# Kernel optimization log

Hardware: AMD Instinct MI355X
Metric: run time of the kernel (lower is better)

## Reference

```python
import jax, jax.numpy as jnp
import numpy as np


def setup_inputs() -> dict:
    key = jax.random.key(0)
    k1, k2 = jax.random.split(key)
    B, H, W, C = 8, 192, 640, 64
    c1 = jax.random.normal(k1, (B, H, W, C), dtype=jnp.float32)
    warp = jax.random.normal(k2, (B, H, W, C), dtype=jnp.float32)
    return {"c1": c1, "warp": warp, "search_range": 2}


def reference(c1, warp, search_range):
    # c1, warp: [B, H, W, C]; pad warp along width by search_range on both sides
    padded = jnp.pad(warp, ((0, 0), (0, 0), (search_range, search_range), (0, 0)))
    width = c1.shape[2]
    max_offset = 2 * search_range + 1  # small fixed loop (5 offsets)
    cost_vol = [
        jnp.mean(c1 * padded[:, :, i:width + i, :], axis=3, keepdims=True)
        for i in range(max_offset)
    ]
    # cost_curve: [B, H, W, C + max_offset]
    return jnp.concatenate([c1] + cost_vol, axis=3)
```

## Files before the change

### kernel.cpp

```cpp
#include <hip/hip_runtime.h>


typedef float f32x4 __attribute__((ext_vector_type(4)));

#define WIDTH 640
#define CH 64
#define NOFF 5
#define OUTC 69
#define GPX 4
#define REC_F4 ((GPX * OUTC) / 4)
#define NPIX (8 * 192 * 640)
#define NGROUPS (NPIX / GPX)
#define BDIM 256
#define WPB (BDIM / 64)
#define GPW 2
#define NBLOCKS (NGROUPS / (WPB * GPW))
#define GROUPS_PER_ROW (WIDTH / GPX)

__device__ __forceinline__ float row_reduce_sum16_lane0(float v) {
    union { float f; int i; } a, b;
    a.f = v;
    b.i = __builtin_amdgcn_update_dpp(0, a.i, 0x101, 0xF, 0xF, true); a.f += b.f;
    b.i = __builtin_amdgcn_update_dpp(0, a.i, 0x102, 0xF, 0xF, true); a.f += b.f;
    b.i = __builtin_amdgcn_update_dpp(0, a.i, 0x104, 0xF, 0xF, true); a.f += b.f;
    b.i = __builtin_amdgcn_update_dpp(0, a.i, 0x108, 0xF, 0xF, true); a.f += b.f;
    return a.f;
}

__global__ __launch_bounds__(BDIM) void StereoCostVolume_kernel(
    const float* __restrict__ c1,
    const float* __restrict__ warp,
    float* __restrict__ out)
{
    __shared__ f32x4 lds[WPB * GPW * REC_F4];

    const int t   = threadIdx.x;
    const int wid = t >> 6;
    const int l   = t & 63;
    const int px  = l >> 4;
    const int c4  = l & 15;

    const f32x4* c1f4   = (const f32x4*)c1;
    const f32x4* warpf4 = (const f32x4*)warp;
    f32x4*       outf4  = (f32x4*)out;

    const int gwave = blockIdx.x * WPB + wid;
    const int g0    = gwave * GPW;
    const int row   = g0 / GROUPS_PER_ROW;
    const int gw0   = g0 - row * GROUPS_PER_ROW;

    const int w0 = gw0 * GPX + px;
    const int i0 = (g0 * GPX + px) * 16 + c4;
    const int wb0 = (row * WIDTH + w0) * 16 + c4;

    const f32x4 a0 = __builtin_nontemporal_load(&c1f4[i0]);
    const f32x4 a1 = __builtin_nontemporal_load(&c1f4[i0 + GPX * 16]);

    f32x4 b0[NOFF], b1[NOFF];
    if (gw0 != 0 && gw0 != GROUPS_PER_ROW - 2) {
        #pragma unroll
        for (int d = 0; d < NOFF; ++d) {
            b0[d] = warpf4[wb0 + (d - 2) * 16];
            b1[d] = warpf4[wb0 + (d - 2) * 16 + GPX * 16];
        }
    } else {
        #pragma unroll
        for (int d = 0; d < NOFF; ++d) {
            const int ww0 = w0 + d - 2;
            const int ww1 = ww0 + GPX;
            b0[d] = (ww0 >= 0 && ww0 < WIDTH) ? warpf4[wb0 + (d - 2) * 16]
                                              : f32x4{0.f, 0.f, 0.f, 0.f};
            b1[d] = (ww1 >= 0 && ww1 < WIDTH) ? warpf4[wb0 + (d - 2) * 16 + GPX * 16]
                                              : f32x4{0.f, 0.f, 0.f, 0.f};
        }
    }

    float s0[NOFF], s1[NOFF];
    #pragma unroll
    for (int d = 0; d < NOFF; ++d) {
        const float acc0 = a0.x * b0[d].x + a0.y * b0[d].y + a0.z * b0[d].z + a0.w * b0[d].w;
        const float acc1 = a1.x * b1[d].x + a1.y * b1[d].y + a1.z * b1[d].z + a1.w * b1[d].w;
        s0[d] = row_reduce_sum16_lane0(acc0);
        s1[d] = row_reduce_sum16_lane0(acc1);
    }

    float* rec0 = (float*)&lds[(wid * GPW + 0) * REC_F4];
    float* rec1 = (float*)&lds[(wid * GPW + 1) * REC_F4];
    const int fb = px * OUTC + c4 * 4;
    rec0[fb + 0] = a0.x; rec0[fb + 1] = a0.y; rec0[fb + 2] = a0.z; rec0[fb + 3] = a0.w;
    rec1[fb + 0] = a1.x; rec1[fb + 1] = a1.y; rec1[fb + 2] = a1.z; rec1[fb + 3] = a1.w;
    if (c4 == 0) {
        #pragma unroll
        for (int d = 0; d < NOFF; ++d) {
            rec0[px * OUTC + CH + d] = s0[d] * 0.015625f;
            rec1[px * OUTC + CH + d] = s1[d] * 0.015625f;
        }
    }
    __builtin_amdgcn_wave_barrier();

    {
        const f32x4* r0 = (const f32x4*)rec0;
        const f32x4* r1 = (const f32x4*)rec1;
        const int ob0 = g0 * REC_F4;
        __builtin_nontemporal_store(r0[l], &outf4[ob0 + l]);
        __builtin_nontemporal_store(r1[l], &outf4[ob0 + REC_F4 + l]);
        if (l < REC_F4 - 64) {
            __builtin_nontemporal_store(r0[64 + l], &outf4[ob0 + 64 + l]);
            __builtin_nontemporal_store(r1[64 + l], &outf4[ob0 + REC_F4 + 64 + l]);
        }
    }
}

extern "C" void kernel_launch(void* const* d_in, const int* in_sizes, int n_in,
                              void* d_out, int out_size, void* d_ws, size_t ws_size,
                              hipStream_t stream) {
    const float* c1   = (const float*)d_in[0];
    const float* warp = (const float*)d_in[1];
    float* out = (float*)d_out;

    StereoCostVolume_kernel<<<NBLOCKS, BDIM, 0, stream>>>(c1, warp, out);
}
```

Measured before the change: 126.6 us.

## Make each wave process eight pixel pairs with double-buffered register prefetch

Each wave now loops over eight consecutive 8-pixel groups instead of handling one. It keeps two register fragments so the loads for the next group are issued while the current group is reduced and stored through LDS. The aim is to hide global load latency and amortise per-wave setup and index math. The cost is an eighth of the blocks, which may reduce memory-level parallelism and occupancy, and more registers per thread.

```diff
diff --git a/kernel.cpp b/kernel.cpp
--- a/kernel.cpp
+++ b/kernel.cpp
@@ -7,15 +7,14 @@
 #define CH 64
 #define NOFF 5
 #define OUTC 69
-#define GPX 4
-#define REC_F4 ((GPX * OUTC) / 4)
+#define REC_F4 69
 #define NPIX (8 * 192 * 640)
-#define NGROUPS (NPIX / GPX)
+#define NPAIR (NPIX / 8)
+#define NITER 8
 #define BDIM 256
 #define WPB (BDIM / 64)
-#define GPW 2
-#define NBLOCKS (NGROUPS / (WPB * GPW))
-#define GROUPS_PER_ROW (WIDTH / GPX)
+#define NBLOCKS (NPAIR / (WPB * NITER))
+#define PAIRS_PER_ROW (WIDTH / 8)
 
 __device__ __forceinline__ float row_reduce_sum16_lane0(float v) {
     union { float f; int i; } a, b;
@@ -27,12 +26,17 @@
     return a.f;
 }
 
+struct Frag {
+    f32x4 a0, a1;
+    f32x4 b0[NOFF], b1[NOFF];
+};
+
 __global__ __launch_bounds__(BDIM) void StereoCostVolume_kernel(
     const float* __restrict__ c1,
     const float* __restrict__ warp,
     float* __restrict__ out)
 {
-    __shared__ f32x4 lds[WPB * GPW * REC_F4];
+    __shared__ f32x4 lds[WPB * 2 * REC_F4];
 
     const int t   = threadIdx.x;
     const int wid = t >> 6;
@@ -44,70 +48,87 @@
     const f32x4* warpf4 = (const f32x4*)warp;
     f32x4*       outf4  = (f32x4*)out;
 
-    const int gwave = blockIdx.x * WPB + wid;
-    const int g0    = gwave * GPW;
-    const int row   = g0 / GROUPS_PER_ROW;
-    const int gw0   = g0 - row * GROUPS_PER_ROW;
+    const int wave  = blockIdx.x * WPB + wid;
+    const int pbase = wave * NITER;
+    const int rp0   = pbase % PAIRS_PER_ROW;
+    const bool leftw  = (rp0 == 0);
+    const bool rightw = (rp0 == PAIRS_PER_ROW - NITER);
 
-    const int w0 = gw0 * GPX + px;
-    const int i0 = (g0 * GPX + px) * 16 + c4;
-    const int wb0 = (row * WIDTH + w0) * 16 + c4;
+    const int base0 = (pbase * 8 + px) * 16 + c4;
 
-    const f32x4 a0 = __builtin_nontemporal_load(&c1f4[i0]);
-    const f32x4 a1 = __builtin_nontemporal_load(&c1f4[i0 + GPX * 16]);
+    float* rec0w = (float*)&lds[(wid * 2 + 0) * REC_F4];
+    float* rec1w = (float*)&lds[(wid * 2 + 1) * REC_F4];
+    const f32x4* rec0r = (const f32x4*)rec0w;
+    const f32x4* rec1r = (const f32x4*)rec1w;
 
-    f32x4 b0[NOFF], b1[NOFF];
-    if (gw0 != 0 && gw0 != GROUPS_PER_ROW - 2) {
+    auto LOAD = [&](int it, Frag& F) {
+        const int base = base0 + it * 128;
+        F.a0 = __builtin_nontemporal_load(&c1f4[base]);
+        F.a1 = __builtin_nontemporal_load(&c1f4[base + 64]);
+        const bool edge = (leftw && it == 0) || (rightw && it == NITER - 1);
+        if (!edge) {
+            #pragma unroll
+            for (int d = 0; d < NOFF; ++d) {
+                F.b0[d] = warpf4[base + (d - 2) * 16];
+                F.b1[d] = warpf4[base + 64 + (d - 2) * 16];
+            }
+        } else {
+            const int w0 = (rp0 + it) * 8 + px;
+            #pragma unroll
+            for (int d = 0; d < NOFF; ++d) {
+                const int ww0 = w0 + d - 2;
+                const int ww1 = ww0 + 4;
+                F.b0[d] = (ww0 >= 0 && ww0 < WIDTH) ? warpf4[base + (d - 2) * 16]
+                                                    : f32x4{0.f, 0.f, 0.f, 0.f};
+                F.b1[d] = (ww1 >= 0 && ww1 < WIDTH) ? warpf4[base + 64 + (d - 2) * 16]
+                                                    : f32x4{0.f, 0.f, 0.f, 0.f};
+            }
+        }
+    };
+
+    auto PROC = [&](int it, const Frag& F) {
+        float s0[NOFF], s1[NOFF];
         #pragma unroll
         for (int d = 0; d < NOFF; ++d) {
-            b0[d] = warpf4[wb0 + (d - 2) * 16];
-            b1[d] = warpf4[wb0 + (d - 2) * 16 + GPX * 16];
+            const float acc0 = F.a0.x * F.b0[d].x + F.a0.y * F.b0[d].y
+                             + F.a0.z * F.b0[d].z + F.a0.w * F.b0[d].w;
+            const float acc1 = F.a1.x * F.b1[d].x + F.a1.y * F.b1[d].y
+                             + F.a1.z * F.b1[d].z + F.a1.w * F.b1[d].w;
+            s0[d] = row_reduce_sum16_lane0(acc0);
+            s1[d] = row_reduce_sum16_lane0(acc1);
         }
-    } else {
-        #pragma unroll
-        for (int d = 0; d < NOFF; ++d) {
-            const int ww0 = w0 + d - 2;
-            const int ww1 = ww0 + GPX;
-            b0[d] = (ww0 >= 0 && ww0 < WIDTH) ? warpf4[wb0 + (d - 2) * 16]
-                                              : f32x4{0.f, 0.f, 0.f, 0.f};
-            b1[d] = (ww1 >= 0 && ww1 < WIDTH) ? warpf4[wb0 + (d - 2) * 16 + GPX * 16]
-                                              : f32x4{0.f, 0.f, 0.f, 0.f};
+        const int fb = px * OUTC + c4 * 4;
+        rec0w[fb + 0] = F.a0.x; rec0w[fb + 1] = F.a0.y;
+        rec0w[fb + 2] = F.a0.z; rec0w[fb + 3] = F.a0.w;
+        rec1w[fb + 0] = F.a1.x; rec1w[fb + 1] = F.a1.y;
+        rec1w[fb + 2] = F.a1.z; rec1w[fb + 3] = F.a1.w;
+        if (c4 == 0) {
+            #pragma unroll
+            for (int d = 0; d < NOFF; ++d) {
+                rec0w[px * OUTC + CH + d] = s0[d] * 0.015625f;
+                rec1w[px * OUTC + CH + d] = s1[d] * 0.015625f;
+            }
         }
-    }
+        __builtin_amdgcn_wave_barrier();
 
-    float s0[NOFF], s1[NOFF];
+        const int ob = (pbase + it) * (2 * REC_F4);
+        __builtin_nontemporal_store(rec0r[l], &outf4[ob + l]);
+        __builtin_nontemporal_store(rec1r[l], &outf4[ob + REC_F4 + l]);
+        if (l < REC_F4 - 64) {
+            __builtin_nontemporal_store(rec0r[64 + l], &outf4[ob + 64 + l]);
+            __builtin_nontemporal_store(rec1r[64 + l], &outf4[ob + REC_F4 + 64 + l]);
+        }
+        __builtin_amdgcn_wave_barrier();
+    };
+
+    Frag X, Y;
+    LOAD(0, X);
     #pragma unroll
-    for (int d = 0; d < NOFF; ++d) {
-        const float acc0 = a0.x * b0[d].x + a0.y * b0[d].y + a0.z * b0[d].z + a0.w * b0[d].w;
-        const float acc1 = a1.x * b1[d].x + a1.y * b1[d].y + a1.z * b1[d].z + a1.w * b1[d].w;
-        s0[d] = row_reduce_sum16_lane0(acc0);
-        s1[d] = row_reduce_sum16_lane0(acc1);
-    }
-
-    float* rec0 = (float*)&lds[(wid * GPW + 0) * REC_F4];
-    float* rec1 = (float*)&lds[(wid * GPW + 1) * REC_F4];
-    const int fb = px * OUTC + c4 * 4;
-    rec0[fb + 0] = a0.x; rec0[fb + 1] = a0.y; rec0[fb + 2] = a0.z; rec0[fb + 3] = a0.w;
-    rec1[fb + 0] = a1.x; rec1[fb + 1] = a1.y; rec1[fb + 2] = a1.z; rec1[fb + 3] = a1.w;
-    if (c4 == 0) {
-        #pragma unroll
-        for (int d = 0; d < NOFF; ++d) {
-            rec0[px * OUTC + CH + d] = s0[d] * 0.015625f;
-            rec1[px * OUTC + CH + d] = s1[d] * 0.015625f;
-        }
-    }
-    __builtin_amdgcn_wave_barrier();
-
-    {
-        const f32x4* r0 = (const f32x4*)rec0;
-        const f32x4* r1 = (const f32x4*)rec1;
-        const int ob0 = g0 * REC_F4;
-        __builtin_nontemporal_store(r0[l], &outf4[ob0 + l]);
-        __builtin_nontemporal_store(r1[l], &outf4[ob0 + REC_F4 + l]);
-        if (l < REC_F4 - 64) {
-            __builtin_nontemporal_store(r0[64 + l], &outf4[ob0 + 64 + l]);
-            __builtin_nontemporal_store(r1[64 + l], &outf4[ob0 + REC_F4 + 64 + l]);
-        }
+    for (int ii = 0; ii < NITER; ii += 2) {
+        LOAD(ii + 1, Y);
+        PROC(ii, X);
+        if (ii + 2 < NITER) LOAD(ii + 2, X);
+        PROC(ii + 1, Y);
     }
 }
 
```

New measurement: 125.4 us. About the same (-0.9%).
